# Kernel tuning notes

Hardware: AMD Instinct MI355X
Metric: run time of the kernel (lower is better)

The kernel has to match this reference:

```python
import jax, jax.numpy as jnp
import numpy as np

N1, N2, N3, N4, D = 50000, 100000, 200000, 300000, 256


def setup_inputs() -> dict:
    key = jax.random.key(0)
    ks = jax.random.split(key, 10)
    feat = jax.random.normal(ks[0], (N1, D), dtype=jnp.float32) * 0.5  # scaled so level-4 products stay bounded
    c2a = jax.random.randint(ks[1], (N2,), 0, N1)
    c2b = jax.random.randint(ks[2], (N2,), 0, N1)
    c3a = jax.random.randint(ks[3], (N3,), 0, N2)
    c3b = jax.random.randint(ks[4], (N3,), 0, N2)
    c4a = jax.random.randint(ks[5], (N4,), 0, N3)
    c4b = jax.random.randint(ks[6], (N4,), 0, N3)
    W = jax.random.normal(ks[7], (D, D), dtype=jnp.float32) / jnp.sqrt(jnp.float32(D))
    b = jax.random.normal(ks[8], (D,), dtype=jnp.float32) * 0.01
    return {"feat": feat, "c2a": c2a, "c2b": c2b, "c3a": c3a, "c3b": c3b,
            "c4a": c4a, "c4b": c4b, "W": W, "b": b}


def _scatter_sum(h_parent, ca, cb, num_children):
    # each parent sends its feature to both children; children sum incoming messages
    z = jnp.zeros((num_children, h_parent.shape[1]), dtype=h_parent.dtype)
    return z.at[ca].add(h_parent).at[cb].add(h_parent)


def reference(feat, c2a, c2b, c3a, c3b, c4a, c4b, W, b):
    # upward: prod reduction over the two constituent subpaths (mailbox prod, dim=1)
    h1 = feat
    h2 = h1[c2a] * h1[c2b]            # [N2, D]
    h3 = h2[c3a] * h2[c3b]            # [N3, D]
    h4 = h3[c4a] * h3[c4b]            # [N4, D]
    # downward: sum-scatter parent -> children, h = h + h_down
    h3 = h3 + _scatter_sum(h4, c4a, c4b, h3.shape[0])
    h2 = h2 + _scatter_sum(h3, c3a, c3b, h2.shape[0])
    h1 = h1 + _scatter_sum(h2, c2a, c2b, h1.shape[0])
    # apply_nodes on n1: Linear + SiLU
    out = jax.nn.silu(h1 @ W + b)
    return out
```

## Files before the change

kernel.cpp:

```cpp
#include <hip/hip_runtime.h>
#include <cstdint>
#include <cstddef>

#define DD 256
#define SCAN_BLK 256
#define SCAN_ELEMS 2048

__device__ __forceinline__ float4 ldrow(const float* __restrict__ base, int row, int lane) {
    return ((const float4*)(base + (size_t)row * DD))[lane];
}
__device__ __forceinline__ float4 mul4(float4 a, float4 b) {
    return make_float4(a.x * b.x, a.y * b.y, a.z * b.z, a.w * b.w);
}
__device__ __forceinline__ float4 add4(float4 a, float4 b) {
    return make_float4(a.x + b.x, a.y + b.y, a.z + b.z, a.w + b.w);
}

__global__ void k_count_pairs(const int* __restrict__ ea, const int* __restrict__ eb,
                              int ne, int* __restrict__ cnt) {
    int e = blockIdx.x * blockDim.x + threadIdx.x;
    if (e >= ne) return;
    atomicAdd(&cnt[ea[e]], 1);
    atomicAdd(&cnt[eb[e]], 1);
}

__global__ void k_fill_pairs(const int* __restrict__ ea, const int* __restrict__ eb,
                             int ne, int* __restrict__ cursor, int* __restrict__ ent,
                             int mode) {
    int e = blockIdx.x * blockDim.x + threadIdx.x;
    if (e >= ne) return;
    int a = ea[e], b = eb[e];
    int pa = atomicAdd(&cursor[a], 1);
    int pb = atomicAdd(&cursor[b], 1);
    if (mode == 0) { ent[pa] = e; ent[pb] = e; }
    else           { ent[pa] = b; ent[pb] = a; }
}

__global__ void k_block_sums(const int* __restrict__ cnt, int n, int* __restrict__ bsum) {
    __shared__ int sdata[SCAN_BLK];
    int base = blockIdx.x * SCAN_ELEMS;
    int s = 0;
#pragma unroll
    for (int k = 0; k < 8; ++k) {
        int idx = base + threadIdx.x + k * SCAN_BLK;
        if (idx < n) s += cnt[idx];
    }
    sdata[threadIdx.x] = s;
    __syncthreads();
    for (int off = SCAN_BLK / 2; off > 0; off >>= 1) {
        if (threadIdx.x < off) sdata[threadIdx.x] += sdata[threadIdx.x + off];
        __syncthreads();
    }
    if (threadIdx.x == 0) bsum[blockIdx.x] = sdata[0];
}

__global__ void k_scan_bsums(int* __restrict__ bsum, int nb, int* __restrict__ total_out) {
    if (threadIdx.x == 0 && blockIdx.x == 0) {
        int acc = 0;
        for (int b = 0; b < nb; ++b) { int v = bsum[b]; bsum[b] = acc; acc += v; }
        *total_out = acc;
    }
}

__global__ void k_scan_final(const int* __restrict__ cnt, int n,
                             const int* __restrict__ bsum, int* __restrict__ offs) {
    __shared__ int sdata[SCAN_BLK];
    int base = blockIdx.x * SCAN_ELEMS;
    int t0 = base + threadIdx.x * 8;
    int loc[8];
    int s = 0;
#pragma unroll
    for (int k = 0; k < 8; ++k) {
        int idx = t0 + k;
        int v = (idx < n) ? cnt[idx] : 0;
        loc[k] = s;
        s += v;
    }
    sdata[threadIdx.x] = s;
    __syncthreads();
    int run = s;
    for (int off = 1; off < SCAN_BLK; off <<= 1) {
        int add = (threadIdx.x >= (unsigned)off) ? sdata[threadIdx.x - off] : 0;
        __syncthreads();
        run += add;
        sdata[threadIdx.x] = run;
        __syncthreads();
    }
    int texcl = run - s + bsum[blockIdx.x];
#pragma unroll
    for (int k = 0; k < 8; ++k) {
        int idx = t0 + k;
        if (idx < n) offs[idx] = texcl + loc[k];
    }
}

__global__ void k_h2(const float* __restrict__ feat, const int* __restrict__ c2a,
                     const int* __restrict__ c2b, float* __restrict__ h2, int n2) {
    int q = blockIdx.x * 4 + (threadIdx.x >> 6);
    int lane = threadIdx.x & 63;
    if (q >= n2) return;
    float4 v = mul4(ldrow(feat, c2a[q], lane), ldrow(feat, c2b[q], lane));
    ((float4*)(h2 + (size_t)q * DD))[lane] = v;
}

__global__ void k_h3tot_h2(const float* __restrict__ h2,
                           const int* __restrict__ c3a, const int* __restrict__ c3b,
                           const int* __restrict__ offs4, const int* __restrict__ ent4,
                           float* __restrict__ h3chunk, int lo, int hi) {
    int j = lo + blockIdx.x * 4 + (threadIdx.x >> 6);
    int lane = threadIdx.x & 63;
    if (j >= hi) return;
    float4 own = mul4(ldrow(h2, c3a[j], lane), ldrow(h2, c3b[j], lane));
    float4 s = make_float4(0.f, 0.f, 0.f, 0.f);
    int e0 = offs4[j], e1 = offs4[j + 1];
    for (int e = e0; e < e1; ++e) {
        int o = ent4[e];
        s = add4(s, mul4(ldrow(h2, c3a[o], lane), ldrow(h2, c3b[o], lane)));
    }
    float4 r = mul4(own, make_float4(1.f + s.x, 1.f + s.y, 1.f + s.z, 1.f + s.w));
    ((float4*)(h3chunk + (size_t)(j - lo) * DD))[lane] = r;
}

__global__ void k_h1_pass(const float* __restrict__ feat,
                          const float* __restrict__ h2,
                          const int* __restrict__ offs3, const int* __restrict__ ent3,
                          const int* __restrict__ offs2, const int* __restrict__ ent2,
                          const float* __restrict__ h3chunk,
                          float* __restrict__ out, int n1, int lo, int hi, int first) {
    int i = blockIdx.x * 4 + (threadIdx.x >> 6);
    int lane = threadIdx.x & 63;
    if (i >= n1) return;
    float4 h = first ? ldrow(feat, i, lane) : ldrow(out, i, lane);
    int e0 = offs2[i], e1 = offs2[i + 1];
    for (int e = e0; e < e1; ++e) {
        int q = ent2[e];
        if (first) h = add4(h, ldrow(h2, q, lane));
        int f0 = offs3[q], f1 = offs3[q + 1];
        for (int f = f0; f < f1; ++f) {
            int j = ent3[f];
            if (j >= lo && j < hi)
                h = add4(h, ldrow(h3chunk, j - lo, lane));
        }
    }
    ((float4*)(out + (size_t)i * DD))[lane] = h;
}

__global__ void k_h3tot_feat(const float* __restrict__ feat,
                             const int* __restrict__ c2a, const int* __restrict__ c2b,
                             const int* __restrict__ c3a, const int* __restrict__ c3b,
                             const int* __restrict__ offs4, const int* __restrict__ ent4,
                             float* __restrict__ h3tot, int n3) {
    int j = blockIdx.x * 4 + (threadIdx.x >> 6);
    int lane = threadIdx.x & 63;
    if (j >= n3) return;
    int q1 = c3a[j], q2 = c3b[j];
    float4 own = mul4(mul4(ldrow(feat, c2a[q1], lane), ldrow(feat, c2b[q1], lane)),
                      mul4(ldrow(feat, c2a[q2], lane), ldrow(feat, c2b[q2], lane)));
    float4 s = make_float4(0.f, 0.f, 0.f, 0.f);
    int e0 = offs4[j], e1 = offs4[j + 1];
    for (int e = e0; e < e1; ++e) {
        int o = ent4[e];
        int p1 = c3a[o], p2 = c3b[o];
        float4 ho = mul4(mul4(ldrow(feat, c2a[p1], lane), ldrow(feat, c2b[p1], lane)),
                         mul4(ldrow(feat, c2a[p2], lane), ldrow(feat, c2b[p2], lane)));
        s = add4(s, ho);
    }
    float4 r = mul4(own, make_float4(1.f + s.x, 1.f + s.y, 1.f + s.z, 1.f + s.w));
    ((float4*)(h3tot + (size_t)j * DD))[lane] = r;
}

__global__ void k_h1_feat(const float* __restrict__ feat,
                          const int* __restrict__ c2a, const int* __restrict__ c2b,
                          const int* __restrict__ offs3, const int* __restrict__ ent3,
                          const int* __restrict__ offs2, const int* __restrict__ ent2,
                          const float* __restrict__ h3tot, float* __restrict__ out, int n1) {
    int i = blockIdx.x * 4 + (threadIdx.x >> 6);
    int lane = threadIdx.x & 63;
    if (i >= n1) return;
    float4 h = ldrow(feat, i, lane);
    int e0 = offs2[i], e1 = offs2[i + 1];
    for (int e = e0; e < e1; ++e) {
        int q = ent2[e];
        float4 acc = mul4(ldrow(feat, c2a[q], lane), ldrow(feat, c2b[q], lane));
        int f0 = offs3[q], f1 = offs3[q + 1];
        for (int f = f0; f < f1; ++f)
            acc = add4(acc, ldrow(h3tot, ent3[f], lane));
        h = add4(h, acc);
    }
    ((float4*)(out + (size_t)i * DD))[lane] = h;
}

__device__ __forceinline__ float silu_f(float x) { return x / (1.0f + expf(-x)); }

__global__ __launch_bounds__(256) void k_gemm_silu(float* __restrict__ h,
                                                   const float* __restrict__ W,
                                                   const float* __restrict__ bias,
                                                   int n1) {
    __shared__ float As[32 * DD];
    const int t = threadIdx.x;
    const int row0 = blockIdx.x * 32;

    const float4* hv = (const float4*)h;
    float4* As4 = (float4*)As;
#pragma unroll
    for (int i = 0; i < 8; ++i) {
        int idx = t + i * 256;
        int r = idx >> 6, c = idx & 63;
        int gr = row0 + r;
        float4 v = make_float4(0.f, 0.f, 0.f, 0.f);
        if (gr < n1) v = hv[(size_t)gr * 64 + c];
        As4[idx] = v;
    }
    __syncthreads();

    const int rg = t >> 6;
    const int cg = t & 63;
    const float4* Wv = (const float4*)W;

    float4 acc[8];
#pragma unroll
    for (int r = 0; r < 8; ++r) acc[r] = make_float4(0.f, 0.f, 0.f, 0.f);

    for (int k = 0; k < DD; k += 4) {
        float4 a[8];
#pragma unroll
        for (int r = 0; r < 8; ++r)
            a[r] = *(const float4*)&As[(rg * 8 + r) * DD + k];
#pragma unroll
        for (int kk = 0; kk < 4; ++kk) {
            float4 w = Wv[(size_t)(k + kk) * 64 + cg];
#pragma unroll
            for (int r = 0; r < 8; ++r) {
                float av = (kk == 0) ? a[r].x : (kk == 1) ? a[r].y
                         : (kk == 2) ? a[r].z : a[r].w;
                acc[r].x += av * w.x;
                acc[r].y += av * w.y;
                acc[r].z += av * w.z;
                acc[r].w += av * w.w;
            }
        }
    }

    float4 bb = ((const float4*)bias)[cg];
    float4* ho = (float4*)h;
#pragma unroll
    for (int r = 0; r < 8; ++r) {
        int gr = row0 + rg * 8 + r;
        if (gr >= n1) continue;
        float4 x = acc[r];
        x.x = silu_f(x.x + bb.x);
        x.y = silu_f(x.y + bb.y);
        x.z = silu_f(x.z + bb.z);
        x.w = silu_f(x.w + bb.w);
        ho[(size_t)gr * 64 + cg] = x;
    }
}

static inline size_t al16(size_t x) { return (x + 15) & ~(size_t)15; }

extern "C" void kernel_launch(void* const* d_in, const int* in_sizes, int n_in,
                              void* d_out, int out_size, void* d_ws, size_t ws_size,
                              hipStream_t stream) {
    const float* feat = (const float*)d_in[0];
    const int* c2a = (const int*)d_in[1];
    const int* c2b = (const int*)d_in[2];
    const int* c3a = (const int*)d_in[3];
    const int* c3b = (const int*)d_in[4];
    const int* c4a = (const int*)d_in[5];
    const int* c4b = (const int*)d_in[6];
    const float* W = (const float*)d_in[7];
    const float* bias = (const float*)d_in[8];

    const int N1 = in_sizes[0] / DD;
    const int N2 = in_sizes[1];
    const int N3 = in_sizes[3];
    const int N4 = in_sizes[5];
    float* out = (float*)d_out;
    char* ws = (char*)d_ws;

    dim3 blk(256);
    auto rows_grid = [](int n) { return dim3((unsigned)((n + 3) / 4)); };
    auto thr_grid = [](int n) { return dim3((unsigned)((n + 255) / 256)); };

    int maxN = N1 > N2 ? N1 : N2;
    if (N3 > maxN) maxN = N3;

    size_t cnt_b = al16((size_t)maxN * 4);
    size_t bsum_b = al16(1024);
    size_t offs4_b = al16((size_t)(N3 + 1) * 4);
    size_t ent4_b = al16((size_t)2 * N4 * 4);
    size_t offs3_b = al16((size_t)(N2 + 1) * 4);
    size_t ent3_b = al16((size_t)2 * N3 * 4);
    size_t offs2_b = al16((size_t)(N1 + 1) * 4);
    size_t ent2_b = al16((size_t)2 * N2 * 4);
    size_t csr_b = cnt_b + bsum_b + offs4_b + ent4_b + offs3_b + ent3_b +
                   offs2_b + ent2_b;
    size_t h2_b = (size_t)N2 * DD * sizeof(float);
    size_t h3_b = (size_t)N3 * DD * sizeof(float);

    char* p = ws;
    int* cnt = (int*)p;    p += cnt_b;
    int* bsum = (int*)p;   p += bsum_b;
    int* offs4 = (int*)p;  p += offs4_b;
    int* ent4 = (int*)p;   p += ent4_b;
    int* offs3 = (int*)p;  p += offs3_b;
    int* ent3 = (int*)p;   p += ent3_b;
    int* offs2 = (int*)p;  p += offs2_b;
    int* ent2 = (int*)p;   p += ent2_b;
    char* dyn = p;

    auto build_csr = [&](const int* ea, const int* eb, int ne, int nnode,
                         int* offs, int* ent, int mode) {
        hipMemsetAsync(cnt, 0, (size_t)nnode * 4, stream);
        k_count_pairs<<<thr_grid(ne), blk, 0, stream>>>(ea, eb, ne, cnt);
        int nb = (nnode + SCAN_ELEMS - 1) / SCAN_ELEMS;
        k_block_sums<<<dim3((unsigned)nb), dim3(SCAN_BLK), 0, stream>>>(cnt, nnode, bsum);
        k_scan_bsums<<<dim3(1), dim3(64), 0, stream>>>(bsum, nb, offs + nnode);
        k_scan_final<<<dim3((unsigned)nb), dim3(SCAN_BLK), 0, stream>>>(cnt, nnode, bsum, offs);
        hipMemcpyAsync(cnt, offs, (size_t)nnode * 4, hipMemcpyDeviceToDevice, stream);
        k_fill_pairs<<<thr_grid(ne), blk, 0, stream>>>(ea, eb, ne, cnt, ent, mode);
    };

    size_t free_after_h2 = (ws_size > csr_b + h2_b) ? ws_size - csr_b - h2_b : 0;
    int chunk_rows = (int)(free_after_h2 / ((size_t)DD * sizeof(float)));
    if (chunk_rows > N3) chunk_rows = N3;

    if (chunk_rows >= 25000) {
        float* h2 = (float*)dyn;
        float* h3chunk = (float*)(dyn + h2_b);

        build_csr(c4a, c4b, N4, N3, offs4, ent4, 1);
        build_csr(c3a, c3b, N3, N2, offs3, ent3, 0);
        build_csr(c2a, c2b, N2, N1, offs2, ent2, 0);

        k_h2<<<rows_grid(N2), blk, 0, stream>>>(feat, c2a, c2b, h2, N2);

        int first = 1;
        for (int lo = 0; lo < N3; lo += chunk_rows) {
            int hi = lo + chunk_rows;
            if (hi > N3) hi = N3;
            k_h3tot_h2<<<rows_grid(hi - lo), blk, 0, stream>>>(h2, c3a, c3b,
                                                               offs4, ent4,
                                                               h3chunk, lo, hi);
            k_h1_pass<<<rows_grid(N1), blk, 0, stream>>>(feat, h2, offs3, ent3,
                                                         offs2, ent2, h3chunk,
                                                         out, N1, lo, hi, first);
            first = 0;
        }
    } else if (ws_size >= csr_b + h3_b) {
        float* h3tot = (float*)dyn;
        build_csr(c4a, c4b, N4, N3, offs4, ent4, 1);
        build_csr(c3a, c3b, N3, N2, offs3, ent3, 0);
        build_csr(c2a, c2b, N2, N1, offs2, ent2, 0);
        k_h3tot_feat<<<rows_grid(N3), blk, 0, stream>>>(feat, c2a, c2b, c3a, c3b,
                                                        offs4, ent4, h3tot, N3);
        k_h1_feat<<<rows_grid(N1), blk, 0, stream>>>(feat, c2a, c2b, offs3, ent3,
                                                     offs2, ent2, h3tot, out, N1);
    }

    k_gemm_silu<<<dim3((unsigned)((N1 + 31) / 32)), blk, 0, stream>>>(out, W, bias, N1);
}
```

Baseline: 902.5 us.

## Flatten two-hop CSR, prefetch grandparent pairs, and split h1 init from chunk passes

Builds a flattened level-1 to level-3 adjacency (entF) so each h1 chunk pass walks one list instead of a nested loop. The level-4 CSR now stores the (c3a, c3b) pair of each sibling directly, which removes a dependent index load in the h3 kernel. The h2 contribution to out moves into a separate init kernel, and the gather loops are unrolled by two to expose more memory parallelism. The fallback path that recomputed products from feat is removed, and the extra index arrays use more workspace, which can shrink chunk_rows.

```diff
diff --git a/kernel.cpp b/kernel.cpp
--- a/kernel.cpp
+++ b/kernel.cpp
@@ -24,16 +24,29 @@
     atomicAdd(&cnt[eb[e]], 1);
 }
 
-__global__ void k_fill_pairs(const int* __restrict__ ea, const int* __restrict__ eb,
-                             int ne, int* __restrict__ cursor, int* __restrict__ ent,
-                             int mode) {
+__global__ void k_fill_edges(const int* __restrict__ ea, const int* __restrict__ eb,
+                             int ne, int* __restrict__ cursor, int* __restrict__ ent) {
     int e = blockIdx.x * blockDim.x + threadIdx.x;
     if (e >= ne) return;
     int a = ea[e], b = eb[e];
     int pa = atomicAdd(&cursor[a], 1);
     int pb = atomicAdd(&cursor[b], 1);
-    if (mode == 0) { ent[pa] = e; ent[pb] = e; }
-    else           { ent[pa] = b; ent[pb] = a; }
+    ent[pa] = e;
+    ent[pb] = e;
+}
+
+__global__ void k_fill_pairs4(const int* __restrict__ c4a, const int* __restrict__ c4b,
+                              const int* __restrict__ c3a, const int* __restrict__ c3b,
+                              int ne, int* __restrict__ cursor, int2* __restrict__ entp) {
+    int e = blockIdx.x * blockDim.x + threadIdx.x;
+    if (e >= ne) return;
+    int a = c4a[e], b = c4b[e];
+    int2 prA = make_int2(c3a[b], c3b[b]);
+    int2 prB = make_int2(c3a[a], c3b[a]);
+    int pa = atomicAdd(&cursor[a], 1);
+    int pb = atomicAdd(&cursor[b], 1);
+    entp[pa] = prA;
+    entp[pb] = prB;
 }
 
 __global__ void k_block_sums(const int* __restrict__ cnt, int n, int* __restrict__ bsum) {
@@ -94,6 +107,33 @@
     }
 }
 
+__global__ void k_flat_cnt(const int* __restrict__ offs2, const int* __restrict__ ent2,
+                           const int* __restrict__ offs3, int n1, int* __restrict__ cntF) {
+    int i = blockIdx.x * blockDim.x + threadIdx.x;
+    if (i >= n1) return;
+    int c = 0;
+    int e0 = offs2[i], e1 = offs2[i + 1];
+    for (int e = e0; e < e1; ++e) {
+        int q = ent2[e];
+        c += offs3[q + 1] - offs3[q];
+    }
+    cntF[i] = c;
+}
+
+__global__ void k_flat_fill(const int* __restrict__ offs2, const int* __restrict__ ent2,
+                            const int* __restrict__ offs3, const int* __restrict__ ent3,
+                            const int* __restrict__ offsF, int n1, int* __restrict__ entF) {
+    int i = blockIdx.x * blockDim.x + threadIdx.x;
+    if (i >= n1) return;
+    int pos = offsF[i];
+    int e0 = offs2[i], e1 = offs2[i + 1];
+    for (int e = e0; e < e1; ++e) {
+        int q = ent2[e];
+        int f0 = offs3[q], f1 = offs3[q + 1];
+        for (int f = f0; f < f1; ++f) entF[pos++] = ent3[f];
+    }
+}
+
 __global__ void k_h2(const float* __restrict__ feat, const int* __restrict__ c2a,
                      const int* __restrict__ c2b, float* __restrict__ h2, int n2) {
     int q = blockIdx.x * 4 + (threadIdx.x >> 6);
@@ -103,9 +143,27 @@
     ((float4*)(h2 + (size_t)q * DD))[lane] = v;
 }
 
+__global__ void k_out_init(const float* __restrict__ feat, const float* __restrict__ h2,
+                           const int* __restrict__ offs2, const int* __restrict__ ent2,
+                           float* __restrict__ out, int n1) {
+    int i = blockIdx.x * 4 + (threadIdx.x >> 6);
+    int lane = threadIdx.x & 63;
+    if (i >= n1) return;
+    float4 h = ldrow(feat, i, lane);
+    int e0 = offs2[i], e1 = offs2[i + 1];
+    int e = e0;
+    for (; e + 1 < e1; e += 2) {
+        int q0 = ent2[e], q1 = ent2[e + 1];
+        float4 v0 = ldrow(h2, q0, lane), v1 = ldrow(h2, q1, lane);
+        h = add4(h, add4(v0, v1));
+    }
+    if (e < e1) h = add4(h, ldrow(h2, ent2[e], lane));
+    ((float4*)(out + (size_t)i * DD))[lane] = h;
+}
+
 __global__ void k_h3tot_h2(const float* __restrict__ h2,
                            const int* __restrict__ c3a, const int* __restrict__ c3b,
-                           const int* __restrict__ offs4, const int* __restrict__ ent4,
+                           const int* __restrict__ offs4, const int2* __restrict__ entp,
                            float* __restrict__ h3chunk, int lo, int hi) {
     int j = lo + blockIdx.x * 4 + (threadIdx.x >> 6);
     int lane = threadIdx.x & 63;
@@ -113,79 +171,47 @@
     float4 own = mul4(ldrow(h2, c3a[j], lane), ldrow(h2, c3b[j], lane));
     float4 s = make_float4(0.f, 0.f, 0.f, 0.f);
     int e0 = offs4[j], e1 = offs4[j + 1];
-    for (int e = e0; e < e1; ++e) {
-        int o = ent4[e];
-        s = add4(s, mul4(ldrow(h2, c3a[o], lane), ldrow(h2, c3b[o], lane)));
+    int e = e0;
+    for (; e + 1 < e1; e += 2) {
+        int2 p0 = entp[e], p1 = entp[e + 1];
+        float4 a0 = ldrow(h2, p0.x, lane), b0 = ldrow(h2, p0.y, lane);
+        float4 a1 = ldrow(h2, p1.x, lane), b1 = ldrow(h2, p1.y, lane);
+        s = add4(s, add4(mul4(a0, b0), mul4(a1, b1)));
+    }
+    if (e < e1) {
+        int2 p = entp[e];
+        s = add4(s, mul4(ldrow(h2, p.x, lane), ldrow(h2, p.y, lane)));
     }
     float4 r = mul4(own, make_float4(1.f + s.x, 1.f + s.y, 1.f + s.z, 1.f + s.w));
     ((float4*)(h3chunk + (size_t)(j - lo) * DD))[lane] = r;
 }
 
-__global__ void k_h1_pass(const float* __restrict__ feat,
-                          const float* __restrict__ h2,
-                          const int* __restrict__ offs3, const int* __restrict__ ent3,
-                          const int* __restrict__ offs2, const int* __restrict__ ent2,
+__global__ void k_h1_flat(const int* __restrict__ offsF, const int* __restrict__ entF,
                           const float* __restrict__ h3chunk,
-                          float* __restrict__ out, int n1, int lo, int hi, int first) {
+                          float* __restrict__ out, int n1, int lo, int hi) {
     int i = blockIdx.x * 4 + (threadIdx.x >> 6);
     int lane = threadIdx.x & 63;
     if (i >= n1) return;
-    float4 h = first ? ldrow(feat, i, lane) : ldrow(out, i, lane);
-    int e0 = offs2[i], e1 = offs2[i + 1];
-    for (int e = e0; e < e1; ++e) {
-        int q = ent2[e];
-        if (first) h = add4(h, ldrow(h2, q, lane));
-        int f0 = offs3[q], f1 = offs3[q + 1];
-        for (int f = f0; f < f1; ++f) {
-            int j = ent3[f];
-            if (j >= lo && j < hi)
-                h = add4(h, ldrow(h3chunk, j - lo, lane));
+    float4 h = ldrow(out, i, lane);
+    int f0 = offsF[i], f1 = offsF[i + 1];
+    int f = f0;
+    for (; f + 1 < f1; f += 2) {
+        int j0 = entF[f], j1 = entF[f + 1];
+        bool in0 = (j0 >= lo) && (j0 < hi);
+        bool in1 = (j1 >= lo) && (j1 < hi);
+        if (in0 && in1) {
+            float4 v0 = ldrow(h3chunk, j0 - lo, lane);
+            float4 v1 = ldrow(h3chunk, j1 - lo, lane);
+            h = add4(h, add4(v0, v1));
+        } else if (in0) {
+            h = add4(h, ldrow(h3chunk, j0 - lo, lane));
+        } else if (in1) {
+            h = add4(h, ldrow(h3chunk, j1 - lo, lane));
         }
     }
-    ((float4*)(out + (size_t)i * DD))[lane] = h;
-}
-
-__global__ void k_h3tot_feat(const float* __restrict__ feat,
-                             const int* __restrict__ c2a, const int* __restrict__ c2b,
-                             const int* __restrict__ c3a, const int* __restrict__ c3b,
-                             const int* __restrict__ offs4, const int* __restrict__ ent4,
-                             float* __restrict__ h3tot, int n3) {
-    int j = blockIdx.x * 4 + (threadIdx.x >> 6);
-    int lane = threadIdx.x & 63;
-    if (j >= n3) return;
-    int q1 = c3a[j], q2 = c3b[j];
-    float4 own = mul4(mul4(ldrow(feat, c2a[q1], lane), ldrow(feat, c2b[q1], lane)),
-                      mul4(ldrow(feat, c2a[q2], lane), ldrow(feat, c2b[q2], lane)));
-    float4 s = make_float4(0.f, 0.f, 0.f, 0.f);
-    int e0 = offs4[j], e1 = offs4[j + 1];
-    for (int e = e0; e < e1; ++e) {
-        int o = ent4[e];
-        int p1 = c3a[o], p2 = c3b[o];
-        float4 ho = mul4(mul4(ldrow(feat, c2a[p1], lane), ldrow(feat, c2b[p1], lane)),
-                         mul4(ldrow(feat, c2a[p2], lane), ldrow(feat, c2b[p2], lane)));
-        s = add4(s, ho);
-    }
-    float4 r = mul4(own, make_float4(1.f + s.x, 1.f + s.y, 1.f + s.z, 1.f + s.w));
-    ((float4*)(h3tot + (size_t)j * DD))[lane] = r;
-}
-
-__global__ void k_h1_feat(const float* __restrict__ feat,
-                          const int* __restrict__ c2a, const int* __restrict__ c2b,
-                          const int* __restrict__ offs3, const int* __restrict__ ent3,
-                          const int* __restrict__ offs2, const int* __restrict__ ent2,
-                          const float* __restrict__ h3tot, float* __restrict__ out, int n1) {
-    int i = blockIdx.x * 4 + (threadIdx.x >> 6);
-    int lane = threadIdx.x & 63;
-    if (i >= n1) return;
-    float4 h = ldrow(feat, i, lane);
-    int e0 = offs2[i], e1 = offs2[i + 1];
-    for (int e = e0; e < e1; ++e) {
-        int q = ent2[e];
-        float4 acc = mul4(ldrow(feat, c2a[q], lane), ldrow(feat, c2b[q], lane));
-        int f0 = offs3[q], f1 = offs3[q + 1];
-        for (int f = f0; f < f1; ++f)
-            acc = add4(acc, ldrow(h3tot, ent3[f], lane));
-        h = add4(h, acc);
+    if (f < f1) {
+        int j0 = entF[f];
+        if (j0 >= lo && j0 < hi) h = add4(h, ldrow(h3chunk, j0 - lo, lane));
     }
     ((float4*)(out + (size_t)i * DD))[lane] = h;
 }
@@ -285,77 +311,79 @@
     int maxN = N1 > N2 ? N1 : N2;
     if (N3 > maxN) maxN = N3;
 
-    size_t cnt_b = al16((size_t)maxN * 4);
-    size_t bsum_b = al16(1024);
+    size_t cnt_b   = al16((size_t)maxN * 4);
+    size_t bsum_b  = al16(4096);
     size_t offs4_b = al16((size_t)(N3 + 1) * 4);
-    size_t ent4_b = al16((size_t)2 * N4 * 4);
+    size_t entp_b  = al16((size_t)2 * N4 * 8);
     size_t offs3_b = al16((size_t)(N2 + 1) * 4);
-    size_t ent3_b = al16((size_t)2 * N3 * 4);
+    size_t ent3_b  = al16((size_t)2 * N3 * 4);
     size_t offs2_b = al16((size_t)(N1 + 1) * 4);
-    size_t ent2_b = al16((size_t)2 * N2 * 4);
-    size_t csr_b = cnt_b + bsum_b + offs4_b + ent4_b + offs3_b + ent3_b +
-                   offs2_b + ent2_b;
+    size_t ent2_b  = al16((size_t)2 * N2 * 4);
+    size_t offsF_b = al16((size_t)(N1 + 1) * 4);
+    size_t entF_b  = al16((size_t)4 * N3 * 4);
+    size_t fixed_b = cnt_b + bsum_b + offs4_b + entp_b + offs3_b + ent3_b +
+                     offs2_b + ent2_b + offsF_b + entF_b;
     size_t h2_b = (size_t)N2 * DD * sizeof(float);
-    size_t h3_b = (size_t)N3 * DD * sizeof(float);
 
     char* p = ws;
-    int* cnt = (int*)p;    p += cnt_b;
-    int* bsum = (int*)p;   p += bsum_b;
-    int* offs4 = (int*)p;  p += offs4_b;
-    int* ent4 = (int*)p;   p += ent4_b;
-    int* offs3 = (int*)p;  p += offs3_b;
-    int* ent3 = (int*)p;   p += ent3_b;
-    int* offs2 = (int*)p;  p += offs2_b;
-    int* ent2 = (int*)p;   p += ent2_b;
-    char* dyn = p;
-
-    auto build_csr = [&](const int* ea, const int* eb, int ne, int nnode,
-                         int* offs, int* ent, int mode) {
-        hipMemsetAsync(cnt, 0, (size_t)nnode * 4, stream);
-        k_count_pairs<<<thr_grid(ne), blk, 0, stream>>>(ea, eb, ne, cnt);
+    int* cnt   = (int*)p; p += cnt_b;
+    int* bsum  = (int*)p; p += bsum_b;
+    int* offs4 = (int*)p; p += offs4_b;
+    int2* entp = (int2*)p; p += entp_b;
+    int* offs3 = (int*)p; p += offs3_b;
+    int* ent3  = (int*)p; p += ent3_b;
+    int* offs2 = (int*)p; p += offs2_b;
+    int* ent2  = (int*)p; p += ent2_b;
+    int* offsF = (int*)p; p += offsF_b;
+    int* entF  = (int*)p; p += entF_b;
+    float* h2  = (float*)p; p += h2_b;
+    float* h3chunk = (float*)p;
+
+    size_t free_b = (ws_size > fixed_b + h2_b) ? ws_size - fixed_b - h2_b : 0;
+    int chunk_rows = (int)(free_b / ((size_t)DD * sizeof(float)));
+    if (chunk_rows > N3) chunk_rows = N3;
+    if (chunk_rows < 1) chunk_rows = 1;
+    int C = (N3 + chunk_rows - 1) / chunk_rows;
+    chunk_rows = (N3 + C - 1) / C;
+
+    auto scan_offs = [&](int* cn, int nnode, int* offs) {
         int nb = (nnode + SCAN_ELEMS - 1) / SCAN_ELEMS;
-        k_block_sums<<<dim3((unsigned)nb), dim3(SCAN_BLK), 0, stream>>>(cnt, nnode, bsum);
+        k_block_sums<<<dim3((unsigned)nb), dim3(SCAN_BLK), 0, stream>>>(cn, nnode, bsum);
         k_scan_bsums<<<dim3(1), dim3(64), 0, stream>>>(bsum, nb, offs + nnode);
-        k_scan_final<<<dim3((unsigned)nb), dim3(SCAN_BLK), 0, stream>>>(cnt, nnode, bsum, offs);
-        hipMemcpyAsync(cnt, offs, (size_t)nnode * 4, hipMemcpyDeviceToDevice, stream);
-        k_fill_pairs<<<thr_grid(ne), blk, 0, stream>>>(ea, eb, ne, cnt, ent, mode);
+        k_scan_final<<<dim3((unsigned)nb), dim3(SCAN_BLK), 0, stream>>>(cn, nnode, bsum, offs);
     };
 
-    size_t free_after_h2 = (ws_size > csr_b + h2_b) ? ws_size - csr_b - h2_b : 0;
-    int chunk_rows = (int)(free_after_h2 / ((size_t)DD * sizeof(float)));
-    if (chunk_rows > N3) chunk_rows = N3;
-
-    if (chunk_rows >= 25000) {
-        float* h2 = (float*)dyn;
-        float* h3chunk = (float*)(dyn + h2_b);
-
-        build_csr(c4a, c4b, N4, N3, offs4, ent4, 1);
-        build_csr(c3a, c3b, N3, N2, offs3, ent3, 0);
-        build_csr(c2a, c2b, N2, N1, offs2, ent2, 0);
-
-        k_h2<<<rows_grid(N2), blk, 0, stream>>>(feat, c2a, c2b, h2, N2);
-
-        int first = 1;
-        for (int lo = 0; lo < N3; lo += chunk_rows) {
-            int hi = lo + chunk_rows;
-            if (hi > N3) hi = N3;
-            k_h3tot_h2<<<rows_grid(hi - lo), blk, 0, stream>>>(h2, c3a, c3b,
-                                                               offs4, ent4,
-                                                               h3chunk, lo, hi);
-            k_h1_pass<<<rows_grid(N1), blk, 0, stream>>>(feat, h2, offs3, ent3,
-                                                         offs2, ent2, h3chunk,
-                                                         out, N1, lo, hi, first);
-            first = 0;
-        }
-    } else if (ws_size >= csr_b + h3_b) {
-        float* h3tot = (float*)dyn;
-        build_csr(c4a, c4b, N4, N3, offs4, ent4, 1);
-        build_csr(c3a, c3b, N3, N2, offs3, ent3, 0);
-        build_csr(c2a, c2b, N2, N1, offs2, ent2, 0);
-        k_h3tot_feat<<<rows_grid(N3), blk, 0, stream>>>(feat, c2a, c2b, c3a, c3b,
-                                                        offs4, ent4, h3tot, N3);
-        k_h1_feat<<<rows_grid(N1), blk, 0, stream>>>(feat, c2a, c2b, offs3, ent3,
-                                                     offs2, ent2, h3tot, out, N1);
+    hipMemsetAsync(cnt, 0, (size_t)N3 * 4, stream);
+    k_count_pairs<<<thr_grid(N4), blk, 0, stream>>>(c4a, c4b, N4, cnt);
+    scan_offs(cnt, N3, offs4);
+    hipMemcpyAsync(cnt, offs4, (size_t)N3 * 4, hipMemcpyDeviceToDevice, stream);
+    k_fill_pairs4<<<thr_grid(N4), blk, 0, stream>>>(c4a, c4b, c3a, c3b, N4, cnt, entp);
+
+    hipMemsetAsync(cnt, 0, (size_t)N2 * 4, stream);
+    k_count_pairs<<<thr_grid(N3), blk, 0, stream>>>(c3a, c3b, N3, cnt);
+    scan_offs(cnt, N2, offs3);
+    hipMemcpyAsync(cnt, offs3, (size_t)N2 * 4, hipMemcpyDeviceToDevice, stream);
+    k_fill_edges<<<thr_grid(N3), blk, 0, stream>>>(c3a, c3b, N3, cnt, ent3);
+
+    hipMemsetAsync(cnt, 0, (size_t)N1 * 4, stream);
+    k_count_pairs<<<thr_grid(N2), blk, 0, stream>>>(c2a, c2b, N2, cnt);
+    scan_offs(cnt, N1, offs2);
+    hipMemcpyAsync(cnt, offs2, (size_t)N1 * 4, hipMemcpyDeviceToDevice, stream);
+    k_fill_edges<<<thr_grid(N2), blk, 0, stream>>>(c2a, c2b, N2, cnt, ent2);
+
+    k_flat_cnt<<<thr_grid(N1), blk, 0, stream>>>(offs2, ent2, offs3, N1, cnt);
+    scan_offs(cnt, N1, offsF);
+    k_flat_fill<<<thr_grid(N1), blk, 0, stream>>>(offs2, ent2, offs3, ent3, offsF, N1, entF);
+
+    k_h2<<<rows_grid(N2), blk, 0, stream>>>(feat, c2a, c2b, h2, N2);
+    k_out_init<<<rows_grid(N1), blk, 0, stream>>>(feat, h2, offs2, ent2, out, N1);
+
+    for (int lo = 0; lo < N3; lo += chunk_rows) {
+        int hi = lo + chunk_rows;
+        if (hi > N3) hi = N3;
+        k_h3tot_h2<<<rows_grid(hi - lo), blk, 0, stream>>>(h2, c3a, c3b, offs4, entp,
+                                                           h3chunk, lo, hi);
+        k_h1_flat<<<rows_grid(N1), blk, 0, stream>>>(offsF, entF, h3chunk, out, N1, lo, hi);
     }
 
     k_gemm_silu<<<dim3((unsigned)((N1 + 31) / 32)), blk, 0, stream>>>(out, W, bias, N1);
```

Measured after the change: 857.0 us. 1.05x faster.
